# Optimization experiments

Hardware: AMD Instinct MI355X
Metric: run time of the kernel (lower is better)

The kernel has to match this reference:

```python
import jax, jax.numpy as jnp
import numpy as np

B, S, D = 2, 2048, 2048
H = 16
HD = D // H  # 128
ROPE_THETA = 10000.0


def _rotate_half(x):
    # interleaved rotate: [-x2_0, x1_0, -x2_1, x1_1, ...]
    x1 = x[..., ::2]
    x2 = x[..., 1::2]
    return jnp.stack((-x2, x1), axis=-1).reshape(x.shape)


def _rope_cos_sin(seq_len, head_dim, dtype):
    inv_freq = 1.0 / (ROPE_THETA ** (jnp.arange(0, head_dim, 2, dtype=jnp.float32) / head_dim))
    pos = jnp.arange(seq_len, dtype=jnp.float32)
    freqs = pos[:, None] * inv_freq[None, :]          # [S, HD/2]
    angles = jnp.concatenate((freqs, freqs), axis=-1)  # [S, HD]  (matches torch.cat((freqs, freqs), -1))
    return jnp.cos(angles).astype(dtype), jnp.sin(angles).astype(dtype)


def setup_inputs() -> dict:
    key = jax.random.key(0)
    ks = jax.random.split(key, 5)
    scale = 1.0 / np.sqrt(D)
    return {
        "x": jax.random.normal(ks[0], (B, S, D), dtype=jnp.float32),
        "Wq": jax.random.normal(ks[1], (D, D), dtype=jnp.float32) * scale,
        "Wk": jax.random.normal(ks[2], (D, D), dtype=jnp.float32) * scale,
        "Wv": jax.random.normal(ks[3], (D, D), dtype=jnp.float32) * scale,
        "Wo": jax.random.normal(ks[4], (D, D), dtype=jnp.float32) * scale,
    }


def reference(x, Wq, Wk, Wv, Wo):
    b, s, d = x.shape
    # separate Q/K/V projections (no bias), reshape to [B, H, S, HD]
    def proj(W):
        return jnp.einsum('bsd,de->bse', x, W).reshape(b, s, H, HD).transpose(0, 2, 1, 3)
    q, k, v = proj(Wq), proj(Wk), proj(Wv)

    cos, sin = _rope_cos_sin(s, HD, q.dtype)  # [S, HD]
    cos = cos[None, None, :, :]
    sin = sin[None, None, :, :]
    q = q * cos + _rotate_half(q) * sin
    k = k * cos + _rotate_half(k) * sin

    # causal scaled dot-product attention
    scores = jnp.einsum('bhqd,bhkd->bhqk', q, k) / jnp.sqrt(jnp.asarray(HD, q.dtype))
    causal = jnp.tril(jnp.ones((s, s), dtype=bool))
    scores = jnp.where(causal[None, None, :, :], scores, jnp.asarray(-jnp.inf, scores.dtype))
    attn = jax.nn.softmax(scores, axis=-1)
    out = jnp.einsum('bhqk,bhkd->bhqd', attn, v)

    out = out.transpose(0, 2, 1, 3).reshape(b, s, d)
    return jnp.einsum('bsd,de->bse', out, Wo)
```

## Files before the change

### kernel.cpp

```cpp
#include <hip/hip_runtime.h>
#include <hip/hip_bf16.h>
#include <math.h>

typedef unsigned short u16;
typedef unsigned int u32;

#define Bz 2
#define Sz 2048
#define Dz 2048
#define Hz 16
#define HDz 128
#define Mz 4096

typedef __bf16 bf16x8 __attribute__((ext_vector_type(8)));
typedef float f32x4 __attribute__((ext_vector_type(4)));

__device__ __forceinline__ float bf2f(u16 h) {
    union { u32 u; float f; } x; x.u = ((u32)h) << 16; return x.f;
}
__device__ __forceinline__ u16 f2bf(float f) {
    union { float f; u32 u; } x; x.f = f;
    u32 u = x.u;
    return (u16)((u + 0x7FFFu + ((u >> 16) & 1u)) >> 16);
}
__device__ __forceinline__ u32 pack_bf16_trunc(float lo, float hi) {
    union { float f; u32 u; } a, b; a.f = lo; b.f = hi;
    return (a.u >> 16) | (b.u & 0xFFFF0000u);
}
__device__ __forceinline__ u32 pack_bf16_rn(float lo, float hi) {
    return (u32)f2bf(lo) | ((u32)f2bf(hi) << 16);
}
__device__ __forceinline__ float fexp2(float x) {
#if __has_builtin(__builtin_amdgcn_exp2f)
    return __builtin_amdgcn_exp2f(x);
#else
    return exp2f(x);
#endif
}
__device__ __forceinline__ void gl_lds16(const void* g, void* l) {
    __builtin_amdgcn_global_load_lds(
        (const __attribute__((address_space(1))) void*)g,
        (__attribute__((address_space(3))) void*)l, 16, 0, 0);
}

__global__ void cvt_f32_bf16(const float* __restrict__ src, u16* __restrict__ dst) {
    size_t i = (size_t)blockIdx.x * blockDim.x + threadIdx.x;
    float4 a = ((const float4*)src)[2 * i];
    float4 b = ((const float4*)src)[2 * i + 1];
    u16 r[8] = {f2bf(a.x), f2bf(a.y), f2bf(a.z), f2bf(a.w),
                f2bf(b.x), f2bf(b.y), f2bf(b.z), f2bf(b.w)};
    *(uint4*)(dst + 8 * i) = *(const uint4*)r;
}

__global__ void transpose_w(const float* __restrict__ W0, const float* __restrict__ W1,
                            const float* __restrict__ W2, const float* __restrict__ W3,
                            u16* __restrict__ Wt) {
    __shared__ u16 t[64][65];
    const float* src = (blockIdx.z == 0) ? W0 : (blockIdx.z == 1) ? W1
                     : (blockIdx.z == 2) ? W2 : W3;
    u16* dst = Wt + (size_t)blockIdx.z * (Dz * Dz);
    int x = blockIdx.x * 64, y = blockIdx.y * 64;
    int c = threadIdx.x & 63, rb = (threadIdx.x >> 6) * 16;
#pragma unroll
    for (int i = 0; i < 16; i++) {
        int r = rb + i;
        t[r][c] = f2bf(src[(size_t)(y + r) * Dz + x + c]);
    }
    __syncthreads();
#pragma unroll
    for (int i = 0; i < 16; i++) {
        int r = rb + i;
        dst[(size_t)(x + r) * Dz + y + c] = t[c][r];
    }
}

template <int MODE>
__global__ void gemm_bt(const u16* __restrict__ A, const u16* __restrict__ BtBase,
                        void* __restrict__ CBase) {
    const int z = blockIdx.z;
    const u16* Bt = BtBase + (size_t)z * (Dz * Dz);
    const int tid = threadIdx.x, lane = tid & 63, wave = tid >> 6;
    const int ln = lane & 15, qd = lane >> 4;
    const int lid = blockIdx.y * 16 + blockIdx.x;
    const int wid = (lid & 7) * 64 + (lid >> 3);
    const int m0 = (wid >> 4) * 128, n0 = (wid & 15) * 128;

    __shared__ __align__(16) u16 As[128][64];
    __shared__ __align__(16) u16 Bs[128][64];

    f32x4 acc[4][4];
#pragma unroll
    for (int i = 0; i < 4; i++)
#pragma unroll
        for (int j = 0; j < 4; j++) acc[i][j] = (f32x4){0.f, 0.f, 0.f, 0.f};

    const int wm = (wave >> 1) * 64, wn = (wave & 1) * 64;
    const int lr8 = lane >> 3;
    const int bgo = (((lane & 7) ^ lr8) * 8);
    const int x7 = ln & 7;

    for (int k0 = 0; k0 < Dz; k0 += 64) {
        const u16* ga = A  + (size_t)(m0 + wave * 32 + lr8) * Dz + k0 + bgo;
        const u16* gb = Bt + (size_t)(n0 + wave * 32 + lr8) * Dz + k0 + bgo;
#pragma unroll
        for (int i = 0; i < 4; i++) {
            gl_lds16(ga + (size_t)(8 * i) * Dz, &As[wave * 32 + 8 * i][0]);
            gl_lds16(gb + (size_t)(8 * i) * Dz, &Bs[wave * 32 + 8 * i][0]);
        }
        __syncthreads();
#pragma unroll
        for (int kc = 0; kc < 2; kc++) {
            bf16x8 af[4], bff[4];
            const int cs = ((4 * kc + qd) ^ x7) * 8;
#pragma unroll
            for (int i = 0; i < 4; i++) {
                af[i]  = *(const bf16x8*)&As[wm + i * 16 + ln][cs];
                bff[i] = *(const bf16x8*)&Bs[wn + i * 16 + ln][cs];
            }
#pragma unroll
            for (int i = 0; i < 4; i++)
#pragma unroll
                for (int j = 0; j < 4; j++)
                    acc[i][j] = __builtin_amdgcn_mfma_f32_16x16x32_bf16(
                        af[i], bff[j], acc[i][j], 0, 0, 0);
        }
        __syncthreads();
    }

#pragma unroll
    for (int i = 0; i < 4; i++) {
#pragma unroll
        for (int j = 0; j < 4; j++) {
#pragma unroll
            for (int r = 0; r < 4; r++) {
                int row = m0 + wm + i * 16 + qd * 4 + r;
                int col = n0 + wn + j * 16 + ln;
                if (MODE == 0) {
                    ((float*)CBase)[(size_t)row * Dz + col] = acc[i][j][r];
                } else {
                    u16* C = (u16*)CBase + (size_t)z * ((size_t)Mz * Dz);
                    u16 hv = f2bf(acc[i][j][r]);
                    int bb = row >> 11, ss = row & 2047;
                    int hh = col >> 7, hd = col & 127;
                    if (z == 2)
                        C[((size_t)(bb * Hz + hh) * HDz + hd) * Sz + ss] = hv;
                    else
                        C[((size_t)(bb * Hz + hh) * Sz + ss) * HDz + hd] = hv;
                }
            }
        }
    }
}

__global__ void rope_kernel(u16* __restrict__ Q, u16* __restrict__ Kk) {
    u32 idx = blockIdx.x * blockDim.x + threadIdx.x;
    int isK = (idx >> 22) & 1;
    u16* T = isK ? Kk : Q;
    u32 p = idx & 0x3FFFFFu;
    int j = p & 63;
    int s = (p >> 6) & 2047;
    size_t base = (size_t)(p >> 6) * HDz + 2 * j;
    u32 u = *(u32*)(T + base);
    float x0 = bf2f((u16)(u & 0xFFFFu));
    float x1 = bf2f((u16)(u >> 16));
    int i0 = (2 * j) & 63;
    const float LG = 0.20762050593046017f;
    float f0 = exp2f(-LG * (float)i0);
    float f1 = exp2f(-LG * (float)(i0 + 1));
    float th0 = (float)s * f0, th1 = (float)s * f1;
    float s0, c0, s1, c1;
    sincosf(th0, &s0, &c0);
    sincosf(th1, &s1, &c1);
    float scl = isK ? 1.0f : 0.12751771218027603f;
    float y0 = (x0 * c0 - x1 * s0) * scl;
    float y1 = (x1 * c1 + x0 * s1) * scl;
    u32 outw = (u32)f2bf(y0) | ((u32)f2bf(y1) << 16);
    *(u32*)(T + base) = outw;
}

__global__ __launch_bounds__(256, 4)
void flash_attn(const u16* __restrict__ Q, const u16* __restrict__ Kk,
                const u16* __restrict__ Vt, u16* __restrict__ O) {
    const int tid = threadIdx.x, lane = tid & 63, wave = tid >> 6;
    const int ln = lane & 15, qd = lane >> 4;
    const int bh = blockIdx.x & 31;
    const int qt = 31 - (blockIdx.x >> 5);
    const int b = bh >> 4, h = bh & 15;
    const int q0 = qt * 64;
    const u16* Qh = Q  + (size_t)bh * Sz * HDz;
    const u16* Kh = Kk + (size_t)bh * Sz * HDz;
    const u16* Vh = Vt + (size_t)bh * HDz * Sz;

    __shared__ __align__(16) u16 Ks[64][128];
    __shared__ __align__(16) u16 Vs[144][64];

    for (int idx = tid; idx < 16 * 64; idx += 256) {
        int rr = idx >> 6, cc = idx & 63;
        Vs[128 + rr][cc] = (rr == 0) ? (u16)0x3F80 : (u16)0;
    }

    const int qabs = q0 + wave * 16 + ln;
    bf16x8 qf[4];
#pragma unroll
    for (int kc = 0; kc < 4; kc++) {
        uint4 t = *(const uint4*)(Qh + (size_t)qabs * HDz + kc * 32 + qd * 8);
        qf[kc] = *(const bf16x8*)&t;
    }

    float m_run = -INFINITY;
    f32x4 oa[9];
#pragma unroll
    for (int n = 0; n < 9; n++) oa[n] = (f32x4){0.f, 0.f, 0.f, 0.f};

    const int x7 = ln & 7;
    const int l4 = lane >> 4, c16 = lane & 15;
    const int lr8 = lane >> 3;
    const int bgv = ((lane & 7) ^ lr8) * 8;

    for (int k0 = 0; k0 <= q0; k0 += 64) {
        {
#pragma unroll
            for (int i = 0; i < 4; i++) {
                int rw = 4 * (i & 1) + l4;
                const u16* gk = Kh + (size_t)(k0 + 16 * wave + 4 * i + l4) * HDz
                                   + ((c16 ^ rw) * 8);
                gl_lds16(gk, &Ks[16 * wave + 4 * i][0]);
            }
            const u16* gv = Vh + (size_t)(32 * wave + lr8) * Sz + k0 + bgv;
#pragma unroll
            for (int i = 0; i < 4; i++)
                gl_lds16(gv + (size_t)(8 * i) * Sz, &Vs[32 * wave + 8 * i][0]);
        }
        __syncthreads();

        f32x4 sc4[4];
#pragma unroll
        for (int mt = 0; mt < 4; mt++) sc4[mt] = (f32x4){0.f, 0.f, 0.f, 0.f};
#pragma unroll
        for (int kc = 0; kc < 4; kc++) {
            const int cs = ((4 * kc + qd) ^ x7) * 8;
#pragma unroll
            for (int mt = 0; mt < 4; mt++) {
                bf16x8 kf = *(const bf16x8*)&Ks[mt * 16 + ln][cs];
                sc4[mt] = __builtin_amdgcn_mfma_f32_16x16x32_bf16(kf, qf[kc], sc4[mt], 0, 0, 0);
            }
        }
        if (k0 == q0) {
#pragma unroll
            for (int mt = 0; mt < 4; mt++)
#pragma unroll
                for (int r = 0; r < 4; r++)
                    if (mt * 16 + qd * 4 + r > 16 * wave + ln) sc4[mt][r] = -3e38f;
        }

        float rm = -3e38f;
#pragma unroll
        for (int mt = 0; mt < 4; mt++) {
            rm = fmaxf(rm, fmaxf(fmaxf(sc4[mt][0], sc4[mt][1]),
                                 fmaxf(sc4[mt][2], sc4[mt][3])));
        }
        rm = fmaxf(rm, __shfl_xor(rm, 16));
        rm = fmaxf(rm, __shfl_xor(rm, 32));
        float mn = fmaxf(m_run, rm);
        bool resc = (__ballot(mn > m_run) != 0ULL);
        float al = fexp2(m_run - mn);
        m_run = mn;
        if (resc) {
#pragma unroll
            for (int n = 0; n < 9; n++)
#pragma unroll
                for (int r = 0; r < 4; r++) oa[n][r] *= al;
        }

        u32 pku[8];
#pragma unroll
        for (int mt = 0; mt < 4; mt++) {
#pragma unroll
            for (int t = 0; t < 2; t++)
                pku[mt * 2 + t] = pack_bf16_trunc(fexp2(sc4[mt][2 * t] - mn),
                                                  fexp2(sc4[mt][2 * t + 1] - mn));
        }

#pragma unroll
        for (int kc = 0; kc < 2; kc++) {
            union { u32 w[4]; bf16x8 v; } pb;
#pragma unroll
            for (int s = 0; s < 4; s++) {
                int srcl = ((2 * (qd & 1) + (s >> 1)) << 4) | ln;
                u32 a0 = (u32)__shfl((int)pku[4 * kc + (s & 1)], srcl);
                u32 a1 = (u32)__shfl((int)pku[4 * kc + 2 + (s & 1)], srcl);
                pb.w[s] = (qd & 2) ? a1 : a0;
            }
            const int cs = ((4 * kc + qd) ^ x7) * 8;
#pragma unroll
            for (int mt = 0; mt < 9; mt++) {
                bf16x8 vf = *(const bf16x8*)&Vs[mt * 16 + ln][cs];
                oa[mt] = __builtin_amdgcn_mfma_f32_16x16x32_bf16(vf, pb.v, oa[mt], 0, 0, 0);
            }
        }
        __syncthreads();
    }

    float l = __shfl(oa[8][0], ln);
    float linv = 1.0f / l;
    u16* op = O + ((size_t)b * Sz + qabs) * Dz + h * HDz;
#pragma unroll
    for (int mt = 0; mt < 8; mt++) {
        u32 w0 = pack_bf16_rn(oa[mt][0] * linv, oa[mt][1] * linv);
        u32 w1 = pack_bf16_rn(oa[mt][2] * linv, oa[mt][3] * linv);
        uint2 ww; ww.x = w0; ww.y = w1;
        *(uint2*)(op + mt * 16 + qd * 4) = ww;
    }
}

extern "C" void kernel_launch(void* const* d_in, const int* in_sizes, int n_in,
                              void* d_out, int out_size, void* d_ws, size_t ws_size,
                              hipStream_t stream) {
    const float* x  = (const float*)d_in[0];
    const float* Wq = (const float*)d_in[1];
    const float* Wk = (const float*)d_in[2];
    const float* Wv = (const float*)d_in[3];
    const float* Wo = (const float*)d_in[4];
    u16* ws  = (u16*)d_ws;

    u16* wt = ws;
    u16* q  = ws + 16777216;
    u16* kk = q + 8388608;
    u16* v  = kk + 8388608;
    u16* xb = v + 8388608;
    u16* o  = xb;

    cvt_f32_bf16<<<dim3(4096), 256, 0, stream>>>(x, xb);
    transpose_w<<<dim3(32, 32, 4), 256, 0, stream>>>(Wq, Wk, Wv, Wo, wt);
    gemm_bt<1><<<dim3(16, 32, 3), 256, 0, stream>>>(xb, wt, q);
    rope_kernel<<<dim3(32768), 256, 0, stream>>>(q, kk);
    flash_attn<<<dim3(1024), 256, 0, stream>>>(q, kk, v, o);
    gemm_bt<0><<<dim3(16, 32, 1), 256, 0, stream>>>(o, wt + 3 * 4194304, (float*)d_out);
}
```

Measured before the change: 396.2 us.

## Fuse RoPE into QKV GEMM epilogue and reorder attention query tiles

Applies RoPE and the Q softmax scale inside the QKV projection GEMM epilogue, using a lane shuffle to fetch each element's interleaved partner, and drops the standalone rope kernel along with its extra read/write pass over Q and K. It also remaps the flash-attention block index so query tiles are issued in a mixed order (low, high, mid groups) rather than strictly longest-first. The goals are to remove one memory round trip plus a launch, and to balance causal work across CUs. The cost is sincos and exp2 work inside the GEMM epilogue, and the shuffle relies on adjacent lanes holding adjacent columns.

```diff
diff --git a/kernel.cpp b/kernel.cpp
--- a/kernel.cpp
+++ b/kernel.cpp
@@ -139,43 +139,26 @@
                     ((float*)CBase)[(size_t)row * Dz + col] = acc[i][j][r];
                 } else {
                     u16* C = (u16*)CBase + (size_t)z * ((size_t)Mz * Dz);
-                    u16 hv = f2bf(acc[i][j][r]);
+                    float v = acc[i][j][r];
                     int bb = row >> 11, ss = row & 2047;
                     int hh = col >> 7, hd = col & 127;
-                    if (z == 2)
-                        C[((size_t)(bb * Hz + hh) * HDz + hd) * Sz + ss] = hv;
-                    else
-                        C[((size_t)(bb * Hz + hh) * Sz + ss) * HDz + hd] = hv;
+                    if (z == 2) {
+                        C[((size_t)(bb * Hz + hh) * HDz + hd) * Sz + ss] = f2bf(v);
+                    } else {
+                        float partner = __shfl_xor(v, 1);
+                        const float LG = 0.20762050593046017f;
+                        float th = (float)ss * fexp2(-LG * (float)(hd & 63));
+                        float sn, cn;
+                        sincosf(th, &sn, &cn);
+                        float rot = (hd & 1) ? partner : -partner;
+                        float y = v * cn + rot * sn;
+                        if (z == 0) y *= 0.12751771218027603f;
+                        C[((size_t)(bb * Hz + hh) * Sz + ss) * HDz + hd] = f2bf(y);
+                    }
                 }
             }
         }
     }
-}
-
-__global__ void rope_kernel(u16* __restrict__ Q, u16* __restrict__ Kk) {
-    u32 idx = blockIdx.x * blockDim.x + threadIdx.x;
-    int isK = (idx >> 22) & 1;
-    u16* T = isK ? Kk : Q;
-    u32 p = idx & 0x3FFFFFu;
-    int j = p & 63;
-    int s = (p >> 6) & 2047;
-    size_t base = (size_t)(p >> 6) * HDz + 2 * j;
-    u32 u = *(u32*)(T + base);
-    float x0 = bf2f((u16)(u & 0xFFFFu));
-    float x1 = bf2f((u16)(u >> 16));
-    int i0 = (2 * j) & 63;
-    const float LG = 0.20762050593046017f;
-    float f0 = exp2f(-LG * (float)i0);
-    float f1 = exp2f(-LG * (float)(i0 + 1));
-    float th0 = (float)s * f0, th1 = (float)s * f1;
-    float s0, c0, s1, c1;
-    sincosf(th0, &s0, &c0);
-    sincosf(th1, &s1, &c1);
-    float scl = isK ? 1.0f : 0.12751771218027603f;
-    float y0 = (x0 * c0 - x1 * s0) * scl;
-    float y1 = (x1 * c1 + x0 * s1) * scl;
-    u32 outw = (u32)f2bf(y0) | ((u32)f2bf(y1) << 16);
-    *(u32*)(T + base) = outw;
 }
 
 __global__ __launch_bounds__(256, 4)
@@ -184,7 +167,10 @@
     const int tid = threadIdx.x, lane = tid & 63, wave = tid >> 6;
     const int ln = lane & 15, qd = lane >> 4;
     const int bh = blockIdx.x & 31;
-    const int qt = 31 - (blockIdx.x >> 5);
+    const int g = blockIdx.x >> 5;
+    const int gm = g & 7, gj = g >> 3;
+    const int qt = (gj == 0) ? gm : (gj == 1) ? 31 - gm
+                 : (gj == 2) ? 8 + gm : 23 - gm;
     const int b = bh >> 4, h = bh & 15;
     const int q0 = qt * 64;
     const u16* Qh = Q  + (size_t)bh * Sz * HDz;
@@ -333,7 +319,6 @@
     cvt_f32_bf16<<<dim3(4096), 256, 0, stream>>>(x, xb);
     transpose_w<<<dim3(32, 32, 4), 256, 0, stream>>>(Wq, Wk, Wv, Wo, wt);
     gemm_bt<1><<<dim3(16, 32, 3), 256, 0, stream>>>(xb, wt, q);
-    rope_kernel<<<dim3(32768), 256, 0, stream>>>(q, kk);
     flash_attn<<<dim3(1024), 256, 0, stream>>>(q, kk, v, o);
     gemm_bt<0><<<dim3(16, 32, 1), 256, 0, stream>>>(o, wt + 3 * 4194304, (float*)d_out);
 }
```

After: 393.2 us. No clear change (-0.7%).
